# Performance work log

Hardware: AMD Instinct MI355X
Metric: run time of the kernel (lower is better)

The kernel has to match this reference:

```python
import jax, jax.numpy as jnp
import numpy as np

VOCAB, EMBED, HIDDEN = 512, 512, 1024
BATCH, SEQ = 128, 1024


def setup_inputs() -> dict:
    key = jax.random.key(0)
    ks = jax.random.split(key, 9)
    inp = {
        "input_ids": jax.random.randint(ks[0], (BATCH, SEQ), 0, VOCAB),
        "embedding": jax.random.normal(ks[1], (VOCAB, EMBED), dtype=jnp.float32),
        "w_xh0": jax.random.normal(ks[2], (HIDDEN, EMBED), dtype=jnp.float32) * 0.05,
        "w_hh0": jax.random.normal(ks[3], (HIDDEN, HIDDEN), dtype=jnp.float32) * 0.05,
        "b_h0": jnp.zeros((HIDDEN,), dtype=jnp.float32),
        "w_xh1": jax.random.normal(ks[4], (HIDDEN, HIDDEN), dtype=jnp.float32) * 0.05,
        "w_hh1": jax.random.normal(ks[5], (HIDDEN, HIDDEN), dtype=jnp.float32) * 0.05,
        "b_h1": jnp.zeros((HIDDEN,), dtype=jnp.float32),
        "w_hy": jax.random.normal(ks[6], (VOCAB, HIDDEN), dtype=jnp.float32) * 0.05,
        "b_y": jnp.zeros((VOCAB,), dtype=jnp.float32),
    }
    return inp


def reference(input_ids, embedding, w_xh0, w_hh0, b_h0, w_xh1, w_hh1, b_h1, w_hy, b_y):
    # dropout_prob = 0.0 -> dropouts are identity (eval-mode math)
    emb = embedding[input_ids]                # [B, T, E]
    emb_t = jnp.swapaxes(emb, 0, 1)           # [T, B, E] for scan over time
    B = input_ids.shape[0]
    h0_init = jnp.zeros((B, HIDDEN), dtype=embedding.dtype)
    h1_init = jnp.zeros((B, HIDDEN), dtype=embedding.dtype)

    def step(carry, x_t):
        h0, h1 = carry
        h0 = jnp.tanh(x_t @ w_xh0.T + h0 @ w_hh0.T + b_h0)
        h1 = jnp.tanh(h0 @ w_xh1.T + h1 @ w_hh1.T + b_h1)
        logits_t = h1 @ w_hy.T + b_y           # [B, V]
        return (h0, h1), logits_t

    (h0, h1), logits_t = jax.lax.scan(step, (h0_init, h1_init), emb_t)
    logits = jnp.swapaxes(logits_t, 0, 1)      # [B, T, V]
    return logits, h0, h1
```

## Files before the change

kernel.cpp:

```cpp
#include <hip/hip_runtime.h>

#define SEQ_T 1024
#define HID   1024
#define EMB   512
#define VOC   512

typedef _Float16 f16;
typedef _Float16 half8 __attribute__((ext_vector_type(8)));
typedef float floatx4 __attribute__((ext_vector_type(4)));

__device__ __forceinline__ float tanh_fast(float x) {
  float e = __expf(2.0f * x);
  return 1.0f - 2.0f / (e + 1.0f);
}

__device__ __forceinline__ half8 ld_cc(const f16* p) {
  half8 v;
  asm volatile("global_load_dwordx4 %0, %1, off sc0 sc1"
               : "=v"(v) : "v"(p) : "memory");
  return v;
}
__device__ __forceinline__ void st_cc(f16* p, f16 x) {
  unsigned v = (unsigned)__builtin_bit_cast(unsigned short, x);
  asm volatile("global_store_short %0, %1, off sc0 sc1"
               :: "v"(p), "v"(v) : "memory");
}
#define VMCNT(n) asm volatile("s_waitcnt vmcnt(" #n ")" ::: "memory")

__global__ void cvt_f32_f16(const float* __restrict__ src, f16* __restrict__ dst, int n) {
  int i = blockIdx.x * 256 + threadIdx.x;
  if (i < n) dst[i] = (f16)src[i];
}

__global__ __launch_bounds__(256) void phaseA(
    const int* __restrict__ ids, const f16* __restrict__ embh,
    const f16* __restrict__ wxh0h, const float* __restrict__ bh0,
    f16* __restrict__ X0)
{
  int bx = blockIdx.x;
  int mt = bx >> 4, nt = bx & 15;
  int wave = threadIdx.x >> 6, lane = threadIdx.x & 63;
  int m0 = mt * 64 + (wave & 1) * 32;
  int n0 = nt * 64 + (wave >> 1) * 32;
  int l15 = lane & 15, q = lane >> 4;

  int mA = m0 + l15, mB = mA + 16;
  const f16* a0p = embh + (size_t)ids[(mA & 127) * SEQ_T + (mA >> 7)] * EMB + q * 8;
  const f16* a1p = embh + (size_t)ids[(mB & 127) * SEQ_T + (mB >> 7)] * EMB + q * 8;
  const f16* b0p = wxh0h + (size_t)(n0 + l15) * EMB + q * 8;
  const f16* b1p = wxh0h + (size_t)(n0 + 16 + l15) * EMB + q * 8;

  floatx4 acc[2][2] = {};
  for (int k = 0; k < EMB; k += 32) {
    half8 a0 = *(const half8*)(a0p + k);
    half8 a1 = *(const half8*)(a1p + k);
    half8 b0 = *(const half8*)(b0p + k);
    half8 b1 = *(const half8*)(b1p + k);
    acc[0][0] = __builtin_amdgcn_mfma_f32_16x16x32_f16(a0, b0, acc[0][0], 0, 0, 0);
    acc[0][1] = __builtin_amdgcn_mfma_f32_16x16x32_f16(a0, b1, acc[0][1], 0, 0, 0);
    acc[1][0] = __builtin_amdgcn_mfma_f32_16x16x32_f16(a1, b0, acc[1][0], 0, 0, 0);
    acc[1][1] = __builtin_amdgcn_mfma_f32_16x16x32_f16(a1, b1, acc[1][1], 0, 0, 0);
  }
  for (int i = 0; i < 2; i++)
    for (int j = 0; j < 2; j++) {
      int col = n0 + j * 16 + l15;
      float bias = bh0[col];
      for (int e = 0; e < 4; e++) {
        int row = m0 + i * 16 + q * 4 + e;
        X0[(size_t)row * HID + col] = (f16)(acc[i][j][e] + bias);
      }
    }
}

__device__ __forceinline__ void spin_ge(unsigned* p, unsigned tgt) {
  while (__hip_atomic_load(p, __ATOMIC_RELAXED, __HIP_MEMORY_SCOPE_AGENT) < tgt)
    __builtin_amdgcn_s_sleep(1);
}

__global__ __launch_bounds__(256, 1) void rnn_persist(
    const float* __restrict__ whh0, const float* __restrict__ wxh1,
    const float* __restrict__ whh1, const float* __restrict__ bh1,
    const f16* __restrict__ X0, f16* __restrict__ h0buf, f16* __restrict__ h1buf,
    f16* __restrict__ H1, unsigned* __restrict__ cnt)
{
  __shared__ half8 lds[4096];

  const int wg = blockIdx.x;
  const int r = wg >> 4;
  const int c = wg & 15;
  const int wave = threadIdx.x >> 6;
  const int lane = threadIdx.x & 63;
  const int l15 = lane & 15, q = lane >> 4;
  const int r0 = r * 16;
  const int col = c * 64 + wave * 16 + l15;

  unsigned* cA = cnt + r * 64;
  unsigned* cB = cnt + 512 + r * 64;

  half8 wa[32], wbx[32], wbh[32];
  {
    const float* w0 = whh0 + (size_t)col * HID + q * 8;
    const float* w1 = wxh1 + (size_t)col * HID + q * 8;
    const float* w2 = whh1 + (size_t)col * HID + q * 8;
    #pragma unroll
    for (int i = 0; i < 32; i++) {
      const float* p0 = w0 + i * 32;
      const float* p1 = w1 + i * 32;
      const float* p2 = w2 + i * 32;
      #pragma unroll
      for (int j = 0; j < 8; j++) {
        wa[i][j]  = (f16)p0[j];
        wbx[i][j] = (f16)p1[j];
        wbh[i][j] = (f16)p2[j];
      }
    }
  }
  const float bias1 = bh1[col];

  for (int t = 0; t <= SEQ_T; t++) {
    const f16* h0prev  = h0buf + (size_t)(t & 1) * 131072;
    f16*       h0next  = h0buf + (size_t)((t + 1) & 1) * 131072;
    const f16* h1prev2 = h1buf + (size_t)((t + 1) & 1) * 131072;
    f16*       h1new   = h1buf + (size_t)(t & 1) * 131072;

    f16 xv[4];
    if (t < SEQ_T) {
      const f16* x0t = X0 + (size_t)t * 131072;
      #pragma unroll
      for (int e = 0; e < 4; e++)
        xv[e] = x0t[(size_t)(r0 + q * 4 + e) * HID + col];
    }

    if (t >= 1) spin_ge(cA, 64u * t);
    if (t >= 2) spin_ge(cB, 64u * (t - 1));

    const f16* ap0 = h0prev  + (size_t)(r0 + l15) * HID + q * 8;
    const f16* ap1 = h1prev2 + (size_t)(r0 + l15) * HID + q * 8;
    half8 v0[8], v1[8];
    #pragma unroll
    for (int i = 0; i < 8; i++) v0[i] = ld_cc(ap0 + (8 * wave + i) * 32);
    #pragma unroll
    for (int i = 0; i < 8; i++) v1[i] = ld_cc(ap1 + (8 * wave + i) * 32);
    VMCNT(8);
    #pragma unroll
    for (int i = 0; i < 8; i++) lds[(8 * wave + i) * 64 + lane] = v0[i];
    VMCNT(0);
    #pragma unroll
    for (int i = 0; i < 8; i++) lds[2048 + (8 * wave + i) * 64 + lane] = v1[i];
    __syncthreads();

    if (t < SEQ_T) {
      floatx4 a0 = {}, a1 = {};
      #pragma unroll
      for (int i = 0; i < 16; i++) {
        half8 f0 = lds[i * 64 + lane];
        half8 f1 = lds[(16 + i) * 64 + lane];
        a0 = __builtin_amdgcn_mfma_f32_16x16x32_f16(f0, wa[i],      a0, 0, 0, 0);
        a1 = __builtin_amdgcn_mfma_f32_16x16x32_f16(f1, wa[16 + i], a1, 0, 0, 0);
      }
      #pragma unroll
      for (int e = 0; e < 4; e++) {
        int row = r0 + q * 4 + e;
        float vv = a0[e] + a1[e] + (float)xv[e];
        st_cc(h0next + (size_t)row * HID + col, (f16)tanh_fast(vv));
      }
      VMCNT(0);
      if (lane == 0)
        __hip_atomic_fetch_add(cA, 1u, __ATOMIC_RELAXED, __HIP_MEMORY_SCOPE_AGENT);
    }

    if (t >= 1) {
      floatx4 b0 = {}, b1 = {};
      #pragma unroll
      for (int i = 0; i < 32; i++) {
        half8 f0 = lds[i * 64 + lane];
        half8 f1 = lds[2048 + i * 64 + lane];
        b0 = __builtin_amdgcn_mfma_f32_16x16x32_f16(f0, wbx[i], b0, 0, 0, 0);
        b1 = __builtin_amdgcn_mfma_f32_16x16x32_f16(f1, wbh[i], b1, 0, 0, 0);
      }
      f16 hv[4];
      #pragma unroll
      for (int e = 0; e < 4; e++) {
        int row = r0 + q * 4 + e;
        hv[e] = (f16)tanh_fast(b0[e] + b1[e] + bias1);
        st_cc(h1new + (size_t)row * HID + col, hv[e]);
      }
      VMCNT(0);
      if (lane == 0)
        __hip_atomic_fetch_add(cB, 1u, __ATOMIC_RELAXED, __HIP_MEMORY_SCOPE_AGENT);
      f16* h1t = H1 + (size_t)(t - 1) * 131072;
      #pragma unroll
      for (int e = 0; e < 4; e++) {
        int row = r0 + q * 4 + e;
        h1t[(size_t)row * HID + col] = hv[e];
      }
    }
    __syncthreads();
  }
}

__global__ __launch_bounds__(256) void logitsK(
    const f16* __restrict__ H1, const f16* __restrict__ whyh,
    const float* __restrict__ by, float* __restrict__ out)
{
  int bx = blockIdx.x;
  int mt = bx >> 3, nt = bx & 7;
  int wave = threadIdx.x >> 6, lane = threadIdx.x & 63;
  int m0 = mt * 64 + (wave & 1) * 32;
  int n0 = nt * 64 + (wave >> 1) * 32;
  int l15 = lane & 15, q = lane >> 4;

  const f16* a0p = H1 + (size_t)(m0 + l15) * HID + q * 8;
  const f16* a1p = H1 + (size_t)(m0 + 16 + l15) * HID + q * 8;
  const f16* b0p = whyh + (size_t)(n0 + l15) * HID + q * 8;
  const f16* b1p = whyh + (size_t)(n0 + 16 + l15) * HID + q * 8;

  floatx4 acc[2][2] = {};
  for (int k = 0; k < HID; k += 32) {
    half8 a0 = *(const half8*)(a0p + k);
    half8 a1 = *(const half8*)(a1p + k);
    half8 b0 = *(const half8*)(b0p + k);
    half8 b1 = *(const half8*)(b1p + k);
    acc[0][0] = __builtin_amdgcn_mfma_f32_16x16x32_f16(a0, b0, acc[0][0], 0, 0, 0);
    acc[0][1] = __builtin_amdgcn_mfma_f32_16x16x32_f16(a0, b1, acc[0][1], 0, 0, 0);
    acc[1][0] = __builtin_amdgcn_mfma_f32_16x16x32_f16(a1, b0, acc[1][0], 0, 0, 0);
    acc[1][1] = __builtin_amdgcn_mfma_f32_16x16x32_f16(a1, b1, acc[1][1], 0, 0, 0);
  }
  for (int i = 0; i < 2; i++)
    for (int j = 0; j < 2; j++) {
      int col = n0 + j * 16 + l15;
      float bias = by[col];
      for (int e = 0; e < 4; e++) {
        int row = m0 + i * 16 + q * 4 + e;
        int t = row >> 7, b = row & 127;
        out[((size_t)b * SEQ_T + t) * VOC + col] = acc[i][j][e] + bias;
      }
    }
}

__global__ void finals(const f16* __restrict__ h0, const f16* __restrict__ h1,
                       float* __restrict__ out) {
  int i = blockIdx.x * 256 + threadIdx.x;
  out[(size_t)67108864 + i] = (float)h0[i];
  out[(size_t)67108864 + 131072 + i] = (float)h1[i];
}

extern "C" void kernel_launch(void* const* d_in, const int* in_sizes, int n_in,
                              void* d_out, int out_size, void* d_ws, size_t ws_size,
                              hipStream_t stream) {
  const int*   ids  = (const int*)d_in[0];
  const float* emb  = (const float*)d_in[1];
  const float* wxh0 = (const float*)d_in[2];
  const float* whh0 = (const float*)d_in[3];
  const float* bh0  = (const float*)d_in[4];
  const float* wxh1 = (const float*)d_in[5];
  const float* whh1 = (const float*)d_in[6];
  const float* bh1  = (const float*)d_in[7];
  const float* why  = (const float*)d_in[8];
  const float* by   = (const float*)d_in[9];
  float* out = (float*)d_out;

  char* ws = (char*)d_ws;
  f16* embh   = (f16*)(ws + 0);
  f16* wxh0h  = (f16*)(ws + 524288);
  f16* whyh   = (f16*)(ws + 1572864);
  f16* h0buf  = (f16*)(ws + 2621440);
  f16* h1buf  = (f16*)(ws + 3145728);
  unsigned* cnt = (unsigned*)(ws + 3670016);
  f16* X0     = (f16*)(ws + 4194304);
  f16* H1     = (f16*)(ws + 272629760);

  cvt_f32_f16<<<1024, 256, 0, stream>>>(emb,  embh,  262144);
  cvt_f32_f16<<<2048, 256, 0, stream>>>(wxh0, wxh0h, 524288);
  cvt_f32_f16<<<2048, 256, 0, stream>>>(why,  whyh,  524288);
  hipMemsetAsync(ws + 2621440, 0, 1052672, stream);

  phaseA<<<32768, 256, 0, stream>>>(ids, embh, wxh0h, bh0, X0);

  rnn_persist<<<128, 256, 0, stream>>>(whh0, wxh1, whh1, bh1,
                                       X0, h0buf, h1buf, H1, cnt);

  logitsK<<<16384, 256, 0, stream>>>(H1, whyh, by, out);
  finals<<<512, 256, 0, stream>>>(h0buf, h1buf, out);
}
```

Before: 9.962 ms.

## Replace atomic step counters with per-wave flags and a ballot-based poll

Each wave now publishes its progress by writing the step number to its own padded flag slot with a plain coherent store, instead of doing an atomic add on a shared per-row counter. Waiting waves poll all 64 flags of the row group in parallel, one flag per lane, and combine the two layer conditions with a single ballot. The layer-0 flag store is also moved to after the layer-1 MFMA loop, so the h0 store latency is hidden behind compute. This removes atomic contention on a shared counter in the 1024-step serial loop, at the cost of more poll traffic and a later layer-0 signal that could lengthen the critical path.

```diff
diff --git a/kernel.cpp b/kernel.cpp
--- a/kernel.cpp
+++ b/kernel.cpp
@@ -25,7 +25,24 @@
   asm volatile("global_store_short %0, %1, off sc0 sc1"
                :: "v"(p), "v"(v) : "memory");
 }
+__device__ __forceinline__ void st_flag(unsigned* p, unsigned v) {
+  asm volatile("global_store_dword %0, %1, off sc0 sc1"
+               :: "v"(p), "v"(v) : "memory");
+}
 #define VMCNT(n) asm volatile("s_waitcnt vmcnt(" #n ")" ::: "memory")
+
+__device__ __forceinline__ void spin_flags(const unsigned* pA, const unsigned* pB,
+                                           unsigned ta, unsigned tb) {
+  for (;;) {
+    unsigned a, b;
+    asm volatile("global_load_dword %0, %2, off sc0 sc1\n\t"
+                 "global_load_dword %1, %3, off sc0 sc1\n\t"
+                 "s_waitcnt vmcnt(0)"
+                 : "=&v"(a), "=&v"(b) : "v"(pA), "v"(pB) : "memory");
+    if (__ballot((a >= ta) && (b >= tb)) == ~0ull) return;
+    __builtin_amdgcn_s_sleep(1);
+  }
+}
 
 __global__ void cvt_f32_f16(const float* __restrict__ src, f16* __restrict__ dst, int n) {
   int i = blockIdx.x * 256 + threadIdx.x;
@@ -72,16 +89,11 @@
     }
 }
 
-__device__ __forceinline__ void spin_ge(unsigned* p, unsigned tgt) {
-  while (__hip_atomic_load(p, __ATOMIC_RELAXED, __HIP_MEMORY_SCOPE_AGENT) < tgt)
-    __builtin_amdgcn_s_sleep(1);
-}
-
 __global__ __launch_bounds__(256, 1) void rnn_persist(
     const float* __restrict__ whh0, const float* __restrict__ wxh1,
     const float* __restrict__ whh1, const float* __restrict__ bh1,
     const f16* __restrict__ X0, f16* __restrict__ h0buf, f16* __restrict__ h1buf,
-    f16* __restrict__ H1, unsigned* __restrict__ cnt)
+    f16* __restrict__ H1, unsigned* __restrict__ flags)
 {
   __shared__ half8 lds[4096];
 
@@ -94,8 +106,12 @@
   const int r0 = r * 16;
   const int col = c * 64 + wave * 16 + l15;
 
-  unsigned* cA = cnt + r * 64;
-  unsigned* cB = cnt + 512 + r * 64;
+  unsigned* fA = flags + r * 1024;
+  unsigned* fB = flags + 8192 + r * 1024;
+  unsigned* myA = fA + (c * 4 + wave) * 16;
+  unsigned* myB = fB + (c * 4 + wave) * 16;
+  const unsigned* pollA = fA + lane * 16;
+  const unsigned* pollB = fB + lane * 16;
 
   half8 wa[32], wbx[32], wbh[32];
   {
@@ -131,8 +147,8 @@
         xv[e] = x0t[(size_t)(r0 + q * 4 + e) * HID + col];
     }
 
-    if (t >= 1) spin_ge(cA, 64u * t);
-    if (t >= 2) spin_ge(cB, 64u * (t - 1));
+    if (t >= 1)
+      spin_flags(pollA, pollB, (unsigned)t, (unsigned)(t >= 2 ? t - 1 : 0));
 
     const f16* ap0 = h0prev  + (size_t)(r0 + l15) * HID + q * 8;
     const f16* ap1 = h1prev2 + (size_t)(r0 + l15) * HID + q * 8;
@@ -164,13 +180,10 @@
         float vv = a0[e] + a1[e] + (float)xv[e];
         st_cc(h0next + (size_t)row * HID + col, (f16)tanh_fast(vv));
       }
-      VMCNT(0);
-      if (lane == 0)
-        __hip_atomic_fetch_add(cA, 1u, __ATOMIC_RELAXED, __HIP_MEMORY_SCOPE_AGENT);
-    }
-
+    }
+
+    floatx4 b0 = {}, b1 = {};
     if (t >= 1) {
-      floatx4 b0 = {}, b1 = {};
       #pragma unroll
       for (int i = 0; i < 32; i++) {
         half8 f0 = lds[i * 64 + lane];
@@ -178,6 +191,14 @@
         b0 = __builtin_amdgcn_mfma_f32_16x16x32_f16(f0, wbx[i], b0, 0, 0, 0);
         b1 = __builtin_amdgcn_mfma_f32_16x16x32_f16(f1, wbh[i], b1, 0, 0, 0);
       }
+    }
+
+    if (t < SEQ_T) {
+      VMCNT(0);
+      if (lane == 0) st_flag(myA, (unsigned)(t + 1));
+    }
+
+    if (t >= 1) {
       f16 hv[4];
       #pragma unroll
       for (int e = 0; e < 4; e++) {
@@ -186,8 +207,7 @@
         st_cc(h1new + (size_t)row * HID + col, hv[e]);
       }
       VMCNT(0);
-      if (lane == 0)
-        __hip_atomic_fetch_add(cB, 1u, __ATOMIC_RELAXED, __HIP_MEMORY_SCOPE_AGENT);
+      if (lane == 0) st_flag(myB, (unsigned)t);
       f16* h1t = H1 + (size_t)(t - 1) * 131072;
       #pragma unroll
       for (int e = 0; e < 4; e++) {
@@ -266,19 +286,19 @@
   f16* whyh   = (f16*)(ws + 1572864);
   f16* h0buf  = (f16*)(ws + 2621440);
   f16* h1buf  = (f16*)(ws + 3145728);
-  unsigned* cnt = (unsigned*)(ws + 3670016);
+  unsigned* flags = (unsigned*)(ws + 3670016);
   f16* X0     = (f16*)(ws + 4194304);
   f16* H1     = (f16*)(ws + 272629760);
 
   cvt_f32_f16<<<1024, 256, 0, stream>>>(emb,  embh,  262144);
   cvt_f32_f16<<<2048, 256, 0, stream>>>(wxh0, wxh0h, 524288);
   cvt_f32_f16<<<2048, 256, 0, stream>>>(why,  whyh,  524288);
-  hipMemsetAsync(ws + 2621440, 0, 1052672, stream);
+  hipMemsetAsync(ws + 2621440, 0, 1114112, stream);
 
   phaseA<<<32768, 256, 0, stream>>>(ids, embh, wxh0h, bh0, X0);
 
   rnn_persist<<<128, 256, 0, stream>>>(whh0, wxh1, whh1, bh1,
-                                       X0, h0buf, h1buf, H1, cnt);
+                                       X0, h0buf, h1buf, H1, flags);
 
   logitsK<<<16384, 256, 0, stream>>>(H1, whyh, by, out);
   finals<<<512, 256, 0, stream>>>(h0buf, h1buf, out);
```

After: 9.643 ms. 1.03x faster.
